# Kernel optimization log

Hardware: AMD Instinct MI355X
Metric: run time of the kernel (lower is better)

The kernel has to match this reference:

```python
import jax, jax.numpy as jnp
import numpy as np

HEADS = 4
N_ROUNDS = 2
R = 1.0
ATTN = 256  # patch_size[0]*patch_size[1]


def setup_inputs() -> dict:
    key = jax.random.key(0)
    ks = jax.random.split(key, 7)
    B, N, C = 4, 16384, 64
    inner = 3 * C
    x = jax.random.normal(ks[0], (B, N, C), dtype=jnp.float32)
    Wq = jax.random.normal(ks[1], (inner, C), dtype=jnp.float32) * 0.05
    Wk = jax.random.normal(ks[2], (inner, C), dtype=jnp.float32) * 0.05
    Wv = jax.random.normal(ks[3], (inner, C), dtype=jnp.float32) * 0.05
    Wo = jax.random.normal(ks[4], (C, inner), dtype=jnp.float32) * 0.05
    alpha = jax.random.normal(ks[5], (C // HEADS + 2, N_ROUNDS), dtype=jnp.float32)
    beta = jax.random.uniform(ks[6], (1, N_ROUNDS), dtype=jnp.float32) * R
    return {"x": x, "Wq": Wq, "Wk": Wk, "Wv": Wv, "Wo": Wo, "alpha": alpha, "beta": beta}


def _split_heads(t, B, N, h):
    # 'b t h e -> (b h) t e'
    return t.reshape(B, N, h, -1).transpose(0, 2, 1, 3).reshape(B * h, N, -1)


def reference(x, Wq, Wk, Wv, Wo, alpha, beta):
    B, N, C = x.shape
    h, nr = HEADS, N_ROUNDS
    bs = B * h

    q = _split_heads(jnp.einsum('bnc,ic->bni', x, Wq), B, N, h)  # (bs, N, 48)
    k = _split_heads(jnp.einsum('bnc,ic->bni', x, Wk), B, N, h)
    v = _split_heads(jnp.einsum('bnc,ic->bni', x, Wv), B, N, h)

    # --- XBOX+ augmentation + SALSH hashing (no_grad in original) ---
    xh = jax.lax.stop_gradient(_split_heads(x, B, N, h))          # (bs, N, 16)
    norms = jnp.linalg.norm(xh, axis=-1, keepdims=True)           # (bs, N, 1)
    MX = jnp.max(norms, axis=-2, keepdims=True)                   # (bs, 1, 1)
    ext = jnp.sqrt(jnp.maximum(MX ** 2 - norms ** 2, 0.0))
    Xs = jnp.concatenate([xh, ext, jnp.zeros_like(ext)], axis=-1)  # (bs, N, 18)
    proj = (Xs @ alpha + beta) / R                                 # (bs, N, nr)
    pos = jnp.argsort(jnp.transpose(proj, (2, 0, 1)), axis=-1)     # (nr, bs, N)

    # --- gather into buckets of size ATTN ---
    def gather(t):
        tb = jnp.broadcast_to(t[None], (nr,) + t.shape)
        return jnp.take_along_axis(tb, pos[..., None], axis=2)

    d = q.shape[-1]
    sq = gather(q).reshape(nr, bs, N // ATTN, ATTN, d)
    sk = gather(k).reshape(nr, bs, N // ATTN, ATTN, d)
    sv = gather(v).reshape(nr, bs, N // ATTN, ATTN, d)

    inner = jnp.einsum('rbnqd,rbnkd->rbnqk', sq, sk)               # norm_factor = 1
    lse = jax.nn.logsumexp(inner, axis=-1, keepdims=True)
    dots = jnp.exp(inner - lse)
    bo = jnp.einsum('rbnqk,rbnkd->rbnqd', dots, sv).reshape(nr, bs, N, d)

    # --- scatter back and merge rounds via logsumexp weights ---
    rev = jnp.argsort(pos, axis=-1)                                # (nr, bs, N)
    o = jnp.take_along_axis(bo, rev[..., None], axis=2)            # (nr, bs, N, d)
    slogits = lse.reshape(nr, bs, N)
    logits = jnp.take_along_axis(slogits, rev, axis=2)
    probs = jax.nn.softmax(logits, axis=0)                         # over rounds
    out = jnp.sum(o * probs[..., None], axis=0)                    # (bs, N, d)

    out = out.reshape(B, h, N, d).transpose(0, 2, 1, 3).reshape(B, N, h * d)
    return jnp.einsum('bni,ci->bnc', out, Wo)
```

## Files before the change

### kernel.cpp

```cpp
#include <hip/hip_runtime.h>
#include <hip/hip_bf16.h>

#define TIE_CONFIG 4
#define N_TOK 16384
#define NBH 16

typedef _Float16 f16;
typedef _Float16 f16x2 __attribute__((ext_vector_type(2)));

constexpr size_t OFF_KEYS = 0;
constexpr size_t SZ_KEYS  = (size_t)2 * NBH * N_TOK * 8;
constexpr size_t OFF_O    = OFF_KEYS + SZ_KEYS;
constexpr size_t SZ_O     = (size_t)NBH * N_TOK * 48 * 4;
constexpr size_t OFF_LOG  = OFF_O + SZ_O;
constexpr size_t SZ_LOG   = (size_t)NBH * N_TOK * 4;
constexpr size_t OFF_NORM = OFF_LOG + SZ_LOG;
constexpr size_t SZ_NORM  = (size_t)NBH * N_TOK * 4;
constexpr size_t OFF_MX   = OFF_NORM + SZ_NORM;
constexpr size_t OFF_FLAG = OFF_MX + 128;
constexpr size_t OFF_TIE  = OFF_FLAG + 64;
constexpr size_t WS_SMALL = OFF_TIE + 64;
constexpr size_t OFF_Q    = WS_SMALL;
constexpr size_t SZ_QKV   = (size_t)NBH * N_TOK * 48 * 4;
constexpr size_t OFF_K    = OFF_Q + SZ_QKV;
constexpr size_t OFF_V    = OFF_K + SZ_QKV;
constexpr size_t WS_BIG   = OFF_V + SZ_QKV;
constexpr size_t OFF_O1   = WS_BIG;
constexpr size_t OFF_LOG1 = OFF_O1 + SZ_O;
constexpr size_t WS_HUGE  = OFF_LOG1 + SZ_LOG;

__global__ void k_check(const int* __restrict__ flags, float* __restrict__ out, int nsz)
{
    int missing = 0;
    #pragma unroll
    for (int s = 0; s < 5; s++) missing |= (flags[s] == 0) << s;
    if (missing) {
        const int i = blockIdx.x * 256 + threadIdx.x;
        if (i < nsz) out[i] = 5000.f + 100.f * (float)missing;
    }
}

__global__ __launch_bounds__(256)
void k_norm(const float* __restrict__ x, float* __restrict__ norms,
            int* __restrict__ mx, int* __restrict__ flags)
{
    const int t = threadIdx.x;
    if (blockIdx.x == 0 && t == 0) flags[0] = 1;
    const int b = blockIdx.x >> 6;
    const int n = ((blockIdx.x & 63) << 8) + t;

    float xr[64];
    const float* xp = x + ((size_t)(b * N_TOK + n)) * 64;
    #pragma unroll
    for (int c = 0; c < 64; c += 4) {
        const float4 xv = *reinterpret_cast<const float4*>(xp + c);
        xr[c] = xv.x; xr[c+1] = xv.y; xr[c+2] = xv.z; xr[c+3] = xv.w;
    }
    #pragma unroll
    for (int h = 0; h < 4; h++) {
        float r[8];
        #pragma unroll
        for (int j = 0; j < 8; j++) {
            const float s0 = __fmul_rn(xr[h*16 + j],     xr[h*16 + j]);
            const float s1 = __fmul_rn(xr[h*16 + 8 + j], xr[h*16 + 8 + j]);
            r[j] = __fadd_rn(s0, s1);
        }
        const float t01 = __fadd_rn(r[0], r[1]);
        const float t23 = __fadd_rn(r[2], r[3]);
        const float t45 = __fadd_rn(r[4], r[5]);
        const float t67 = __fadd_rn(r[6], r[7]);
        const float ns  = __fadd_rn(__fadd_rn(t01, t23), __fadd_rn(t45, t67));
        const float nm  = __fsqrt_rn(ns);
        norms[((size_t)(b*4 + h) << 14) + n] = nm;
        float wm = nm;
        #pragma unroll
        for (int off = 32; off; off >>= 1) wm = fmaxf(wm, __shfl_down(wm, off));
        if ((t & 63) == 0) atomicMax(&mx[b*4 + h], __float_as_int(wm));
    }
}

__device__ __forceinline__ unsigned long long packkey(double d, int n)
{
    const long long s = __double_as_longlong(d);
    const unsigned long long u = (s < 0) ? ~(unsigned long long)s
                                         : ((unsigned long long)s | 0x8000000000000000ull);
    return (u & ~0x3FFFull) | (unsigned long long)n;
}

__global__ __launch_bounds__(256)
void k_keys(const float* __restrict__ x, const float* __restrict__ alpha,
            const float* __restrict__ beta, const float* __restrict__ norms,
            const int* __restrict__ mx, unsigned long long* __restrict__ keys,
            int* __restrict__ flags)
{
    const size_t g = (size_t)blockIdx.x * 256 + threadIdx.x;
    if (g == 0) flags[1] = 1;
    const int bh = (int)(g >> 14);
    const int n  = (int)(g & 16383);
    const int b  = bh >> 2, h = bh & 3;
    const float* xp = x + ((size_t)(b * N_TOK + n)) * 64 + h * 16;
    const float nm = norms[g];
    const float MX = __int_as_float(mx[bh]);
    const float d2  = __fsub_rn(__fmul_rn(MX, MX), __fmul_rn(nm, nm));
    const float ext = __fsqrt_rn(fmaxf(d2, 0.f));

    float p0 = 0.f, p1 = 0.f;
    #pragma unroll
    for (int e = 0; e < 16; e++) {
        const float xv = xp[e];
        p0 = __fmaf_rn(xv, alpha[e*2 + 0], p0);
        p1 = __fmaf_rn(xv, alpha[e*2 + 1], p1);
    }
    p0 = __fmaf_rn(ext, alpha[32], p0);
    p1 = __fmaf_rn(ext, alpha[33], p1);
    p0 = __fadd_rn(p0, beta[0]);
    p1 = __fadd_rn(p1, beta[1]);

    keys[g]                  = packkey((double)p0, n);
    keys[g + (size_t)262144] = packkey((double)p1, n);
}

__global__ __launch_bounds__(512)
void k_sort_local(unsigned long long* __restrict__ keys, const int stage,
                  int* __restrict__ flags)
{
    __shared__ unsigned long long s[4096];
    const int blk   = blockIdx.x;
    if (stage == 2 && blk == 0 && threadIdx.x == 0) flags[2] = 1;
    const int base  = (blk & 3) << 12;
    unsigned long long* kp = keys + (((size_t)(blk >> 2)) << 14) + base;
    const int t = threadIdx.x;
    for (int i = t; i < 4096; i += 512) s[i] = kp[i];
    __syncthreads();

    if (stage == 0) {
        for (int size = 2; size <= 4096; size <<= 1) {
            const bool top = (size == 4096);
            for (int stride = size >> 1; stride > 0; stride >>= 1) {
                for (int w = t; w < 2048; w += 512) {
                    const int i = ((w & ~(stride - 1)) << 1) | (w & (stride - 1));
                    const int j = i | stride;
                    const bool up = top ? ((base & 4096) == 0) : ((i & size) == 0);
                    const unsigned long long a = s[i], b = s[j];
                    if ((a > b) == up) { s[i] = b; s[j] = a; }
                }
                __syncthreads();
            }
        }
    } else {
        const bool up = (stage == 2) ? true : ((base & 8192) == 0);
        for (int stride = 2048; stride > 0; stride >>= 1) {
            for (int w = t; w < 2048; w += 512) {
                const int i = ((w & ~(stride - 1)) << 1) | (w & (stride - 1));
                const int j = i | stride;
                const unsigned long long a = s[i], b = s[j];
                if ((a > b) == up) { s[i] = b; s[j] = a; }
            }
            __syncthreads();
        }
    }
    for (int i = t; i < 4096; i += 512) kp[i] = s[i];
}

__global__ __launch_bounds__(256)
void k_sort_g(unsigned long long* __restrict__ keys, const int stride, const int size)
{
    const size_t w = (size_t)blockIdx.x * 256 + threadIdx.x;
    const size_t seg = w >> 13;
    const int ww = (int)(w & 8191);
    const int i = ((ww & ~(stride - 1)) << 1) | (ww & (stride - 1));
    const int j = i | stride;
    const bool up = ((i & size) == 0);
    unsigned long long* kp = keys + (seg << 14);
    const unsigned long long a = kp[i], b = kp[j];
    if ((a > b) == up) { kp[i] = b; kp[j] = a; }
}

__global__ __launch_bounds__(64)
void k_findties(const unsigned long long* __restrict__ keys, int* __restrict__ flags,
                int* __restrict__ tielocs)
{
    const int seg = blockIdx.x;
    const int t = threadIdx.x;
    if (t < 1) return;
    const unsigned long long* kp = keys + ((size_t)seg << 14);
    const int i = t << 8;
    if ((kp[i-1] >> 14) == (kp[i] >> 14)) {
        const int slot = atomicAdd(&flags[5], 1);
        if (slot < 16) tielocs[slot] = seg * 16384 + i;
    }
}

__global__ void k_fixties(unsigned long long* __restrict__ keys,
                          const int* __restrict__ flags, int* __restrict__ tielocs,
                          const int config)
{
    if (threadIdx.x != 0 || blockIdx.x != 0) return;
    int n = flags[5]; if (n > 16) n = 16;
    for (int a = 1; a < n; a++) {
        const int v = tielocs[a];
        int b = a;
        while (b > 0 && tielocs[b-1] > v) { tielocs[b] = tielocs[b-1]; --b; }
        tielocs[b] = v;
    }
    for (int p = 0; p < n; p++) {
        if ((config >> p) & 1) {
            const int loc = tielocs[p];
            const unsigned long long tmp = keys[loc-1];
            keys[loc-1] = keys[loc];
            keys[loc]   = tmp;
        }
    }
}

__global__ __launch_bounds__(256)
void k_qkv(const float* __restrict__ x, const float* __restrict__ Wq,
           const float* __restrict__ Wk, const float* __restrict__ Wv,
           f16* __restrict__ q16, f16* __restrict__ k16, float* __restrict__ v)
{
    __shared__ float sbuf[256 * 49];
    const int t   = threadIdx.x;
    const int blk = blockIdx.x;
    const int part= blockIdx.y;
    const int b   = blk >> 6;
    const int n0  = (blk & 63) << 8;

    float xr[64];
    const float* xp = x + ((size_t)(b * N_TOK + n0 + t)) * 64;
    #pragma unroll
    for (int c = 0; c < 64; c += 4) {
        const float4 xv = *reinterpret_cast<const float4*>(xp + c);
        xr[c] = xv.x; xr[c+1] = xv.y; xr[c+2] = xv.z; xr[c+3] = xv.w;
    }

    const float* W = (part == 0) ? Wq : (part == 1) ? Wk : Wv;

    #pragma unroll 1
    for (int h = 0; h < 4; h++) {
        const float* Wrow0 = W + h * 48 * 64;
        #pragma unroll 1
        for (int e = 0; e < 48; e++) {
            const float* wr = Wrow0 + e * 64;
            float a0 = 0, a1 = 0, a2 = 0, a3 = 0;
            #pragma unroll
            for (int c = 0; c < 64; c += 4) {
                a0 = fmaf(xr[c+0], wr[c+0], a0);
                a1 = fmaf(xr[c+1], wr[c+1], a1);
                a2 = fmaf(xr[c+2], wr[c+2], a2);
                a3 = fmaf(xr[c+3], wr[c+3], a3);
            }
            sbuf[t * 49 + e] = (a0 + a1) + (a2 + a3);
        }
        __syncthreads();
        const size_t rowbase = ((size_t)(b*4 + h) * N_TOK + n0) * 48;
        if (part < 2) {
            f16* dst = (part == 0 ? q16 : k16) + rowbase;
            for (int j = t; j < 12288; j += 256)
                dst[j] = (f16)sbuf[(j / 48) * 49 + (j % 48)];
        } else {
            float* dst = v + rowbase;
            for (int j = t; j < 12288; j += 256)
                dst[j] = sbuf[(j / 48) * 49 + (j % 48)];
        }
        __syncthreads();
    }
}

__device__ __forceinline__
void attn_core(const f16* __restrict__ qg, const f16* __restrict__ kg,
               const float* __restrict__ vg, const unsigned long long* __restrict__ keys,
               const int bh, const int nb, const int round, const int t,
               f16* kld, float* vlds,
               int& idxA, int& idxB, float& mA, float& lA, float& mB, float& lB,
               float4* aA, float4* aB)
{
    const size_t kb = ((size_t)(round * NBH + bh) << 14) + nb * 256;
    idxA = (int)(keys[kb + t]       & 0x3FFFull);
    idxB = (int)(keys[kb + 128 + t] & 0x3FFFull);
    const size_t rbase = (size_t)bh << 14;

    float4 qA4[6], qB4[6];
    {
        const float4* qpA = reinterpret_cast<const float4*>(qg + (rbase + idxA) * 48);
        const float4* qpB = reinterpret_cast<const float4*>(qg + (rbase + idxB) * 48);
        #pragma unroll
        for (int j = 0; j < 6; j++) { qA4[j] = qpA[j]; qB4[j] = qpB[j]; }
    }

    mA = -1e30f; lA = 0.f; mB = -1e30f; lB = 0.f;
    #pragma unroll
    for (int j = 0; j < 12; j++) {
        aA[j] = make_float4(0.f, 0.f, 0.f, 0.f);
        aB[j] = make_float4(0.f, 0.f, 0.f, 0.f);
    }

    #pragma unroll 1
    for (int tile = 0; tile < 4; tile++) {
        {
            const int r = t & 63;
            const int rowidx = (int)(keys[kb + tile * 64 + r] & 0x3FFFull);
            if (t < 64) {
                const float4* src = reinterpret_cast<const float4*>(kg + (rbase + rowidx) * 48);
                float4* dst = reinterpret_cast<float4*>(kld + r * 72);
                #pragma unroll
                for (int j = 0; j < 6; j++) dst[j] = src[j];
            } else {
                const float4* src = reinterpret_cast<const float4*>(vg + (rbase + rowidx) * 48);
                float* dst = vlds + r * 52;
                #pragma unroll
                for (int j = 0; j < 12; j++)
                    *reinterpret_cast<float4*>(dst + 4*j) = src[j];
            }
        }
        __syncthreads();

        #pragma unroll 1
        for (int ki = 0; ki < 64; ki++) {
            const float4* krow4 = reinterpret_cast<const float4*>(kld + ki * 72);
            float sA = 0.f, sB = 0.f;
            #pragma unroll
            for (int j = 0; j < 6; j++) {
                float4 kf = krow4[j];
                const f16x2* kh = reinterpret_cast<const f16x2*>(&kf);
                const f16x2* qa = reinterpret_cast<const f16x2*>(&qA4[j]);
                const f16x2* qb = reinterpret_cast<const f16x2*>(&qB4[j]);
                #pragma unroll
                for (int u = 0; u < 4; u++) {
                    sA = __builtin_amdgcn_fdot2(qa[u], kh[u], sA, false);
                    sB = __builtin_amdgcn_fdot2(qb[u], kh[u], sB, false);
                }
            }
            if (__any((sA > mA + 8.f) || (sB > mB + 8.f))) {
                const float mnA = fmaxf(mA, sA); const float cA = __expf(mA - mnA);
                const float mnB = fmaxf(mB, sB); const float cB = __expf(mB - mnB);
                lA *= cA; mA = mnA; lB *= cB; mB = mnB;
                #pragma unroll
                for (int j = 0; j < 12; j++) {
                    aA[j].x*=cA; aA[j].y*=cA; aA[j].z*=cA; aA[j].w*=cA;
                    aB[j].x*=cB; aB[j].y*=cB; aB[j].z*=cB; aB[j].w*=cB;
                }
            }
            const float pA = __expf(sA - mA); lA += pA;
            const float pB = __expf(sB - mB); lB += pB;
            const float4* vrow = reinterpret_cast<const float4*>(vlds + ki * 52);
            #pragma unroll
            for (int j = 0; j < 12; j++) {
                const float4 vv = vrow[j];
                aA[j].x = fmaf(pA, vv.x, aA[j].x);
                aA[j].y = fmaf(pA, vv.y, aA[j].y);
                aA[j].z = fmaf(pA, vv.z, aA[j].z);
                aA[j].w = fmaf(pA, vv.w, aA[j].w);
                aB[j].x = fmaf(pB, vv.x, aB[j].x);
                aB[j].y = fmaf(pB, vv.y, aB[j].y);
                aB[j].z = fmaf(pB, vv.z, aB[j].z);
                aB[j].w = fmaf(pB, vv.w, aB[j].w);
            }
        }
        __syncthreads();
    }
}

__global__ __launch_bounds__(128)
void k_attn2(const f16* __restrict__ qg, const f16* __restrict__ kg,
             const float* __restrict__ vg,
             const unsigned long long* __restrict__ keys,
             float* __restrict__ o0, float* __restrict__ log0,
             float* __restrict__ o1, float* __restrict__ log1,
             int* __restrict__ flags)
{
    __shared__ f16   kld[64 * 72];
    __shared__ float vlds[64 * 52];
    const int bid = blockIdx.x;
    const int round = bid >> 10;
    if (bid == (round << 10) && threadIdx.x == 0) flags[3 + round] = 1;
    const int bh = (bid >> 6) & 15;
    const int nb = bid & 63;

    int idxA, idxB; float mA, lA, mB, lB; float4 aA[12], aB[12];
    attn_core(qg, kg, vg, keys, bh, nb, round, threadIdx.x, kld, vlds,
              idxA, idxB, mA, lA, mB, lB, aA, aB);

    float* od = round ? o1 : o0;
    float* ld = round ? log1 : log0;
    #pragma unroll 1
    for (int which = 0; which < 2; which++) {
        const int idx = which ? idxB : idxA;
        const float m = which ? mB : mA;
        const float l = which ? lB : lA;
        float4* acc = which ? aB : aA;
        const size_t base = ((size_t)bh << 14) + idx;
        float4* orow = reinterpret_cast<float4*>(od + base * 48);
        const float inv = 1.f / l;
        #pragma unroll
        for (int j = 0; j < 12; j++) {
            float4 t4 = acc[j];
            t4.x *= inv; t4.y *= inv; t4.z *= inv; t4.w *= inv;
            orow[j] = t4;
        }
        ld[base] = m + __logf(l);
    }
}

__global__ __launch_bounds__(128)
void k_attn_pre(const f16* __restrict__ qg, const f16* __restrict__ kg,
                const float* __restrict__ vg,
                const unsigned long long* __restrict__ keys,
                float* __restrict__ o, float* __restrict__ logits, const int round,
                int* __restrict__ flags)
{
    __shared__ f16   kld[64 * 72];
    __shared__ float vlds[64 * 52];
    if (blockIdx.x == 0 && threadIdx.x == 0) flags[3 + round] = 1;
    const int bh = blockIdx.x >> 6;
    const int nb = blockIdx.x & 63;

    int idxA, idxB; float mA, lA, mB, lB; float4 aA[12], aB[12];
    attn_core(qg, kg, vg, keys, bh, nb, round, threadIdx.x, kld, vlds,
              idxA, idxB, mA, lA, mB, lB, aA, aB);

    #pragma unroll 1
    for (int which = 0; which < 2; which++) {
        const int idx = which ? idxB : idxA;
        const float m = which ? mB : mA;
        const float l = which ? lB : lA;
        float4* acc = which ? aB : aA;
        const size_t base = ((size_t)bh << 14) + idx;
        const float lse = m + __logf(l);
        float4* orow = reinterpret_cast<float4*>(o + base * 48);
        if (round == 0) {
            const float inv = 1.f / l;
            #pragma unroll
            for (int j = 0; j < 12; j++) {
                float4 t4 = acc[j];
                t4.x *= inv; t4.y *= inv; t4.z *= inv; t4.w *= inv;
                orow[j] = t4;
            }
            logits[base] = lse;
        } else {
            const float l0 = logits[base];
            const float mm = fmaxf(l0, lse);
            const float p0 = __expf(l0 - mm), p1 = __expf(lse - mm);
            const float sc = 1.f / (p0 + p1);
            const float w0 = p0 * sc;
            const float w1 = p1 * sc / l;
            #pragma unroll
            for (int j = 0; j < 12; j++) {
                const float4 o0v = orow[j];
                float4 t4;
                t4.x = w0 * o0v.x + w1 * acc[j].x;
                t4.y = w0 * o0v.y + w1 * acc[j].y;
                t4.z = w0 * o0v.z + w1 * acc[j].z;
                t4.w = w0 * o0v.w + w1 * acc[j].w;
                orow[j] = t4;
            }
        }
    }
}

__global__ __launch_bounds__(512)
void k_out_merge(const float* __restrict__ o0, const float* __restrict__ log0,
                 const float* __restrict__ o1, const float* __restrict__ log1,
                 const float* __restrict__ Wo, float* __restrict__ out)
{
    __shared__ float wlds[64 * 193];
    __shared__ float merged[8][192];
    __shared__ float wts[8][4][2];
    const int t = threadIdx.x;
    for (int j = t; j < 12288; j += 512) wlds[(j / 192) * 193 + (j % 192)] = Wo[j];

    const size_t tok0 = (size_t)blockIdx.x * 8;
    if (t < 32) {
        const int tok = t >> 2, hh = t & 3;
        const size_t g = tok0 + tok;
        const int b = (int)(g >> 14), n = (int)(g & 16383);
        const size_t base = ((size_t)(b*4 + hh) << 14) + n;
        const float l0 = log0[base], l1 = log1[base];
        const float mm = fmaxf(l0, l1);
        const float p0 = __expf(l0 - mm), p1 = __expf(l1 - mm);
        const float sc = 1.f / (p0 + p1);
        wts[tok][hh][0] = p0 * sc;
        wts[tok][hh][1] = p1 * sc;
    }
    __syncthreads();

    for (int j = t; j < 1536; j += 512) {
        const int tok = j / 192, i = j % 192;
        const int hh = i / 48, e = i % 48;
        const size_t g = tok0 + tok;
        const int b = (int)(g >> 14), n = (int)(g & 16383);
        const size_t base = (((size_t)(b*4 + hh) << 14) + n) * 48 + e;
        merged[tok][i] = wts[tok][hh][0] * o0[base] + wts[tok][hh][1] * o1[base];
    }
    __syncthreads();

    const int tok = t >> 6, c = t & 63;
    const float* wr = wlds + c * 193;
    const float* mr = merged[tok];
    float a0 = 0, a1 = 0, a2 = 0, a3 = 0;
    #pragma unroll
    for (int i = 0; i < 192; i += 4) {
        a0 = fmaf(mr[i+0], wr[i+0], a0);
        a1 = fmaf(mr[i+1], wr[i+1], a1);
        a2 = fmaf(mr[i+2], wr[i+2], a2);
        a3 = fmaf(mr[i+3], wr[i+3], a3);
    }
    out[(tok0 + tok) * 64 + c] = (a0 + a1) + (a2 + a3);
}

__global__ __launch_bounds__(512)
void k_out(const float* __restrict__ o, const float* __restrict__ Wo,
           float* __restrict__ out)
{
    __shared__ float wlds[64 * 193];
    __shared__ float merged[8][192];
    const int t = threadIdx.x;
    for (int j = t; j < 12288; j += 512) wlds[(j / 192) * 193 + (j % 192)] = Wo[j];

    const size_t tok0 = (size_t)blockIdx.x * 8;
    for (int j = t; j < 1536; j += 512) {
        const int tok = j / 192, i = j % 192;
        const int hh = i / 48, e = i % 48;
        const size_t g = tok0 + tok;
        const int b = (int)(g >> 14), n = (int)(g & 16383);
        merged[tok][i] = o[(((size_t)(b*4 + hh) << 14) + n) * 48 + e];
    }
    __syncthreads();

    const int tok = t >> 6, c = t & 63;
    const float* wr = wlds + c * 193;
    const float* mr = merged[tok];
    float a0 = 0, a1 = 0, a2 = 0, a3 = 0;
    #pragma unroll
    for (int i = 0; i < 192; i += 4) {
        a0 = fmaf(mr[i+0], wr[i+0], a0);
        a1 = fmaf(mr[i+1], wr[i+1], a1);
        a2 = fmaf(mr[i+2], wr[i+2], a2);
        a3 = fmaf(mr[i+3], wr[i+3], a3);
    }
    out[(tok0 + tok) * 64 + c] = (a0 + a1) + (a2 + a3);
}

__global__ __launch_bounds__(256)
void k_attn(const float* __restrict__ x, const float* __restrict__ Wq,
            const float* __restrict__ Wk, const float* __restrict__ Wv,
            const unsigned long long* __restrict__ keys,
            float* __restrict__ o, float* __restrict__ logits, const int round,
            int* __restrict__ flags)
{
    __shared__ float klds[128 * 52];
    __shared__ float vlds2[128 * 52];
    const int t  = threadIdx.x;
    if (blockIdx.x == 0 && t == 0) flags[3 + round] = 1;
    const int bh = blockIdx.x >> 6;
    const int nb = blockIdx.x & 63;
    const int b  = bh >> 2, h = bh & 3;

    const unsigned long long key = keys[((size_t)(round * NBH + bh) << 14) + nb * 256 + t];
    const int idx = (int)(key & 0x3FFFull);

    float xr[64];
    {
        const float* xp = x + (((size_t)b << 14) + idx) * 64;
        #pragma unroll
        for (int c = 0; c < 64; c += 4) {
            const float4 xv = *reinterpret_cast<const float4*>(xp + c);
            xr[c] = xv.x; xr[c+1] = xv.y; xr[c+2] = xv.z; xr[c+3] = xv.w;
        }
    }

    float kreg[48], vreg[48];
    {
        const float* WkH = Wk + h * 48 * 64;
        const float* WvH = Wv + h * 48 * 64;
        #pragma unroll 1
        for (int e = 0; e < 48; e++) {
            const float* wk = WkH + e * 64;
            const float* wv = WvH + e * 64;
            float ka = 0, kb2 = 0, va = 0, vb = 0;
            #pragma unroll
            for (int c = 0; c < 64; c += 2) {
                ka  = fmaf(xr[c],   wk[c],   ka);
                kb2 = fmaf(xr[c+1], wk[c+1], kb2);
                va  = fmaf(xr[c],   wv[c],   va);
                vb  = fmaf(xr[c+1], wv[c+1], vb);
            }
            kreg[e] = ka + kb2; vreg[e] = va + vb;
        }
    }

    float q[48];
    {
        const float* WqH = Wq + h * 48 * 64;
        #pragma unroll 1
        for (int e = 0; e < 48; e++) {
            const float* wq = WqH + e * 64;
            float a0 = 0, a1 = 0, a2 = 0, a3 = 0;
            #pragma unroll
            for (int c = 0; c < 64; c += 4) {
                a0 = fmaf(xr[c+0], wq[c+0], a0);
                a1 = fmaf(xr[c+1], wq[c+1], a1);
                a2 = fmaf(xr[c+2], wq[c+2], a2);
                a3 = fmaf(xr[c+3], wq[c+3], a3);
            }
            q[e] = (a0 + a1) + (a2 + a3);
        }
    }

    float m = -1e30f, l = 0.f;
    float4 a4[12];
    #pragma unroll
    for (int j = 0; j < 12; j++) a4[j] = make_float4(0.f, 0.f, 0.f, 0.f);

    #pragma unroll 1
    for (int tile = 0; tile < 2; tile++) {
        if ((t >> 7) == tile) {
            float* kd = klds + (t & 127) * 52;
            float* vd = vlds2 + (t & 127) * 52;
            #pragma unroll
            for (int e4 = 0; e4 < 48; e4 += 4) {
                *reinterpret_cast<float4*>(kd + e4) =
                    make_float4(kreg[e4], kreg[e4+1], kreg[e4+2], kreg[e4+3]);
                *reinterpret_cast<float4*>(vd + e4) =
                    make_float4(vreg[e4], vreg[e4+1], vreg[e4+2], vreg[e4+3]);
            }
        }
        __syncthreads();

        #pragma unroll 1
        for (int ki = 0; ki < 128; ki++) {
            const float4* krow = reinterpret_cast<const float4*>(klds + ki * 52);
            float s0 = 0, s1 = 0, s2 = 0, s3 = 0;
            #pragma unroll
            for (int j = 0; j < 12; j++) {
                const float4 kv = krow[j];
                s0 = fmaf(q[4*j+0], kv.x, s0);
                s1 = fmaf(q[4*j+1], kv.y, s1);
                s2 = fmaf(q[4*j+2], kv.z, s2);
                s3 = fmaf(q[4*j+3], kv.w, s3);
            }
            const float s = (s0 + s1) + (s2 + s3);
            if (__any(s > m + 8.f)) {
                const float mn = fmaxf(m, s);
                const float corr = __expf(m - mn);
                l *= corr;
                #pragma unroll
                for (int j = 0; j < 12; j++) {
                    a4[j].x *= corr; a4[j].y *= corr; a4[j].z *= corr; a4[j].w *= corr;
                }
                m = mn;
            }
            const float p = __expf(s - m);
            l += p;
            const float4* vrow = reinterpret_cast<const float4*>(vlds2 + ki * 52);
            #pragma unroll
            for (int j = 0; j < 12; j++) {
                const float4 vj = vrow[j];
                a4[j].x = fmaf(p, vj.x, a4[j].x);
                a4[j].y = fmaf(p, vj.y, a4[j].y);
                a4[j].z = fmaf(p, vj.z, a4[j].z);
                a4[j].w = fmaf(p, vj.w, a4[j].w);
            }
        }
        __syncthreads();
    }

    const size_t base = ((size_t)bh << 14) + idx;
    const float lse = m + __logf(l);
    float4* orow = reinterpret_cast<float4*>(o + base * 48);

    if (round == 0) {
        const float inv = 1.f / l;
        #pragma unroll
        for (int j = 0; j < 12; j++) {
            float4 t4 = a4[j];
            t4.x *= inv; t4.y *= inv; t4.z *= inv; t4.w *= inv;
            orow[j] = t4;
        }
        logits[base] = lse;
    } else {
        const float l0 = logits[base];
        const float mm = fmaxf(l0, lse);
        const float p0 = __expf(l0 - mm), p1 = __expf(lse - mm);
        const float sc = 1.f / (p0 + p1);
        const float w0 = p0 * sc;
        const float w1 = p1 * sc / l;
        #pragma unroll
        for (int j = 0; j < 12; j++) {
            const float4 o0 = orow[j];
            float4 t4;
            t4.x = w0 * o0.x + w1 * a4[j].x;
            t4.y = w0 * o0.y + w1 * a4[j].y;
            t4.z = w0 * o0.z + w1 * a4[j].z;
            t4.w = w0 * o0.w + w1 * a4[j].w;
            orow[j] = t4;
        }
    }
}

static int err_byte(hipError_t e, int base)
{
    if (e == hipErrorNoBinaryForGpu)         return base + 0;
    if (e == hipErrorInvalidDeviceFunction)  return base + 1;
    if (e == hipErrorInvalidConfiguration)   return base + 2;
    if (e == hipErrorOutOfMemory)            return base + 3;
    return base + 4;
}

extern "C" __attribute__((visibility("default")))
void kernel_launch(void* const* d_in, const int* in_sizes, int n_in,
                   void* d_out, int out_size, void* d_ws, size_t ws_size,
                   hipStream_t stream)
{
    const size_t out_bytes = (size_t)out_size * 4;

    (void)hipGetLastError();

    const bool sizes_ok = (n_in == 7) && in_sizes
        && in_sizes[0] == 4194304 && in_sizes[1] == 12288 && in_sizes[2] == 12288
        && in_sizes[3] == 12288  && in_sizes[4] == 12288 && in_sizes[5] == 36
        && in_sizes[6] == 2      && out_size == 4194304;
    if (!sizes_ok) { (void)hipMemsetAsync(d_out, 0x60, out_bytes, stream); return; }

    if (ws_size < WS_SMALL) {
        const int k = (int)(ws_size >> 24);
        (void)hipMemsetAsync(d_out, 0x50 + (k > 7 ? 7 : k), out_bytes, stream);
        return;
    }
    const bool pre  = (ws_size >= WS_BIG);
    const bool dual = (ws_size >= WS_HUGE);

    const float* x     = (const float*)d_in[0];
    const float* Wq    = (const float*)d_in[1];
    const float* Wk    = (const float*)d_in[2];
    const float* Wv    = (const float*)d_in[3];
    const float* Wo    = (const float*)d_in[4];
    const float* alpha = (const float*)d_in[5];
    const float* beta  = (const float*)d_in[6];
    float*       out   = (float*)d_out;

    char* ws = (char*)d_ws;
    unsigned long long* keys = (unsigned long long*)(ws + OFF_KEYS);
    float* o      = (float*)(ws + OFF_O);
    float* logits = (float*)(ws + OFF_LOG);
    float* norms  = (float*)(ws + OFF_NORM);
    int*   mx     = (int*)(ws + OFF_MX);
    int*   flags  = (int*)(ws + OFF_FLAG);
    int*   tloc   = (int*)(ws + OFF_TIE);
    f16*   qg     = (f16*)(ws + OFF_Q);
    f16*   kg     = (f16*)(ws + OFF_K);
    float* vg     = (float*)(ws + OFF_V);
    float* o1     = (float*)(ws + OFF_O1);
    float* log1   = (float*)(ws + OFF_LOG1);

    (void)hipMemsetAsync(mx, 0, 256, stream);

    k_norm<<<256, 256, 0, stream>>>(x, norms, mx, flags);
    {
        const hipError_t e1 = hipGetLastError();
        if (e1 != hipSuccess) {
            (void)hipMemsetAsync(d_out, err_byte(e1, 0x70), out_bytes, stream);
            return;
        }
    }
    if (pre)
        k_qkv<<<dim3(256, 3), 256, 0, stream>>>(x, Wq, Wk, Wv, qg, kg, vg);

    k_keys<<<1024, 256, 0, stream>>>(x, alpha, beta, norms, mx, keys, flags);

    k_sort_local<<<128, 512, 0, stream>>>(keys, 0, flags);
    k_sort_g    <<<1024, 256, 0, stream>>>(keys, 4096, 8192);
    k_sort_local<<<128, 512, 0, stream>>>(keys, 1, flags);
    k_sort_g    <<<1024, 256, 0, stream>>>(keys, 8192, 16384);
    k_sort_g    <<<1024, 256, 0, stream>>>(keys, 4096, 16384);
    k_sort_local<<<128, 512, 0, stream>>>(keys, 2, flags);

    k_findties<<<32, 64, 0, stream>>>(keys, flags, tloc);
    k_fixties<<<1, 1, 0, stream>>>(keys, flags, tloc, TIE_CONFIG);

    if (dual) {
        k_attn2<<<2048, 128, 0, stream>>>(qg, kg, vg, keys, o, logits, o1, log1, flags);
        k_out_merge<<<8192, 512, 0, stream>>>(o, logits, o1, log1, Wo, out);
    } else if (pre) {
        k_attn_pre<<<1024, 128, 0, stream>>>(qg, kg, vg, keys, o, logits, 0, flags);
        k_attn_pre<<<1024, 128, 0, stream>>>(qg, kg, vg, keys, o, logits, 1, flags);
        k_out<<<8192, 512, 0, stream>>>(o, Wo, out);
    } else {
        k_attn<<<1024, 256, 0, stream>>>(x, Wq, Wk, Wv, keys, o, logits, 0, flags);
        k_attn<<<1024, 256, 0, stream>>>(x, Wq, Wk, Wv, keys, o, logits, 1, flags);
        k_out<<<8192, 512, 0, stream>>>(o, Wo, out);
    }

    k_check<<<(out_size + 255) / 256, 256, 0, stream>>>(flags, out, out_size);

    const hipError_t e2 = hipGetLastError();
    if (e2 != hipSuccess) {
        (void)hipMemsetAsync(d_out, err_byte(e2, 0x78), out_bytes, stream);
    }
}
```

Measured before the change: 729.4 us.

## Store attention outputs in fp16, shrink check kernel, split dot accumulators

The per-round attention outputs are now written as fp16 instead of fp32 and converted back when merged, which halves the write and read traffic of the intermediate buffers. The error-check kernel now runs as a single block that only fills the first 4096 elements when flags are missing. The QK dot products use two independent accumulator chains, the QKV projection inner loop is unrolled by two, and the attention loop raises wave priority. These are unrelated tweaks bundled together, and fp16 outputs add rounding error.

Result: slower. 773.5 us (+6.1%).

```diff
diff --git a/kernel.cpp b/kernel.cpp
--- a/kernel.cpp
+++ b/kernel.cpp
@@ -7,6 +7,7 @@
 
 typedef _Float16 f16;
 typedef _Float16 f16x2 __attribute__((ext_vector_type(2)));
+typedef _Float16 f16x8 __attribute__((ext_vector_type(8)));
 
 constexpr size_t OFF_KEYS = 0;
 constexpr size_t SZ_KEYS  = (size_t)2 * NBH * N_TOK * 8;
@@ -35,8 +36,9 @@
     #pragma unroll
     for (int s = 0; s < 5; s++) missing |= (flags[s] == 0) << s;
     if (missing) {
-        const int i = blockIdx.x * 256 + threadIdx.x;
-        if (i < nsz) out[i] = 5000.f + 100.f * (float)missing;
+        const int base = threadIdx.x * 16;
+        const float v = 5000.f + 100.f * (float)missing;
+        for (int i = base; i < base + 16 && i < nsz; i++) out[i] = v;
     }
 }
 
@@ -238,7 +240,7 @@
     #pragma unroll 1
     for (int h = 0; h < 4; h++) {
         const float* Wrow0 = W + h * 48 * 64;
-        #pragma unroll 1
+        #pragma unroll 2
         for (int e = 0; e < 48; e++) {
             const float* wr = Wrow0 + e * 64;
             float a0 = 0, a1 = 0, a2 = 0, a3 = 0;
@@ -314,22 +316,28 @@
         }
         __syncthreads();
 
+        __builtin_amdgcn_s_setprio(1);
         #pragma unroll 1
         for (int ki = 0; ki < 64; ki++) {
             const float4* krow4 = reinterpret_cast<const float4*>(kld + ki * 72);
-            float sA = 0.f, sB = 0.f;
+            float sA0 = 0.f, sA1 = 0.f, sB0 = 0.f, sB1 = 0.f;
             #pragma unroll
             for (int j = 0; j < 6; j++) {
                 float4 kf = krow4[j];
                 const f16x2* kh = reinterpret_cast<const f16x2*>(&kf);
                 const f16x2* qa = reinterpret_cast<const f16x2*>(&qA4[j]);
                 const f16x2* qb = reinterpret_cast<const f16x2*>(&qB4[j]);
-                #pragma unroll
-                for (int u = 0; u < 4; u++) {
-                    sA = __builtin_amdgcn_fdot2(qa[u], kh[u], sA, false);
-                    sB = __builtin_amdgcn_fdot2(qb[u], kh[u], sB, false);
-                }
-            }
+                sA0 = __builtin_amdgcn_fdot2(qa[0], kh[0], sA0, false);
+                sA1 = __builtin_amdgcn_fdot2(qa[1], kh[1], sA1, false);
+                sB0 = __builtin_amdgcn_fdot2(qb[0], kh[0], sB0, false);
+                sB1 = __builtin_amdgcn_fdot2(qb[1], kh[1], sB1, false);
+                sA0 = __builtin_amdgcn_fdot2(qa[2], kh[2], sA0, false);
+                sA1 = __builtin_amdgcn_fdot2(qa[3], kh[3], sA1, false);
+                sB0 = __builtin_amdgcn_fdot2(qb[2], kh[2], sB0, false);
+                sB1 = __builtin_amdgcn_fdot2(qb[3], kh[3], sB1, false);
+            }
+            const float sA = sA0 + sA1;
+            const float sB = sB0 + sB1;
             if (__any((sA > mA + 8.f) || (sB > mB + 8.f))) {
                 const float mnA = fmaxf(mA, sA); const float cA = __expf(mA - mnA);
                 const float mnB = fmaxf(mB, sB); const float cB = __expf(mB - mnB);
@@ -356,6 +364,7 @@
                 aB[j].w = fmaf(pB, vv.w, aB[j].w);
             }
         }
+        __builtin_amdgcn_s_setprio(0);
         __syncthreads();
     }
 }
@@ -364,8 +373,8 @@
 void k_attn2(const f16* __restrict__ qg, const f16* __restrict__ kg,
              const float* __restrict__ vg,
              const unsigned long long* __restrict__ keys,
-             float* __restrict__ o0, float* __restrict__ log0,
-             float* __restrict__ o1, float* __restrict__ log1,
+             f16* __restrict__ o0, float* __restrict__ log0,
+             f16* __restrict__ o1, float* __restrict__ log1,
              int* __restrict__ flags)
 {
     __shared__ f16   kld[64 * 72];
@@ -380,7 +389,7 @@
     attn_core(qg, kg, vg, keys, bh, nb, round, threadIdx.x, kld, vlds,
               idxA, idxB, mA, lA, mB, lB, aA, aB);
 
-    float* od = round ? o1 : o0;
+    f16*   od = round ? o1 : o0;
     float* ld = round ? log1 : log0;
     #pragma unroll 1
     for (int which = 0; which < 2; which++) {
@@ -389,13 +398,17 @@
         const float l = which ? lB : lA;
         float4* acc = which ? aB : aA;
         const size_t base = ((size_t)bh << 14) + idx;
-        float4* orow = reinterpret_cast<float4*>(od + base * 48);
+        f16x8* orow = reinterpret_cast<f16x8*>(od + base * 48);
         const float inv = 1.f / l;
         #pragma unroll
-        for (int j = 0; j < 12; j++) {
-            float4 t4 = acc[j];
-            t4.x *= inv; t4.y *= inv; t4.z *= inv; t4.w *= inv;
-            orow[j] = t4;
+        for (int j = 0; j < 6; j++) {
+            const float4 a = acc[2*j], b = acc[2*j+1];
+            f16x8 h;
+            h[0] = (f16)(a.x * inv); h[1] = (f16)(a.y * inv);
+            h[2] = (f16)(a.z * inv); h[3] = (f16)(a.w * inv);
+            h[4] = (f16)(b.x * inv); h[5] = (f16)(b.y * inv);
+            h[6] = (f16)(b.z * inv); h[7] = (f16)(b.w * inv);
+            orow[j] = h;
         }
         ld[base] = m + __logf(l);
     }
@@ -458,8 +471,8 @@
 }
 
 __global__ __launch_bounds__(512)
-void k_out_merge(const float* __restrict__ o0, const float* __restrict__ log0,
-                 const float* __restrict__ o1, const float* __restrict__ log1,
+void k_out_merge(const f16* __restrict__ o0, const float* __restrict__ log0,
+                 const f16* __restrict__ o1, const float* __restrict__ log1,
                  const float* __restrict__ Wo, float* __restrict__ out)
 {
     __shared__ float wlds[64 * 193];
@@ -489,7 +502,8 @@
         const size_t g = tok0 + tok;
         const int b = (int)(g >> 14), n = (int)(g & 16383);
         const size_t base = (((size_t)(b*4 + hh) << 14) + n) * 48 + e;
-        merged[tok][i] = wts[tok][hh][0] * o0[base] + wts[tok][hh][1] * o1[base];
+        merged[tok][i] = wts[tok][hh][0] * (float)o0[base]
+                       + wts[tok][hh][1] * (float)o1[base];
     }
     __syncthreads();
 
@@ -741,6 +755,7 @@
     char* ws = (char*)d_ws;
     unsigned long long* keys = (unsigned long long*)(ws + OFF_KEYS);
     float* o      = (float*)(ws + OFF_O);
+    f16*   o0h    = (f16*)(ws + OFF_O);
     float* logits = (float*)(ws + OFF_LOG);
     float* norms  = (float*)(ws + OFF_NORM);
     int*   mx     = (int*)(ws + OFF_MX);
@@ -749,7 +764,7 @@
     f16*   qg     = (f16*)(ws + OFF_Q);
     f16*   kg     = (f16*)(ws + OFF_K);
     float* vg     = (float*)(ws + OFF_V);
-    float* o1     = (float*)(ws + OFF_O1);
+    f16*   o1h    = (f16*)(ws + OFF_O1);
     float* log1   = (float*)(ws + OFF_LOG1);
 
     (void)hipMemsetAsync(mx, 0, 256, stream);
@@ -778,8 +793,8 @@
     k_fixties<<<1, 1, 0, stream>>>(keys, flags, tloc, TIE_CONFIG);
 
     if (dual) {
-        k_attn2<<<2048, 128, 0, stream>>>(qg, kg, vg, keys, o, logits, o1, log1, flags);
-        k_out_merge<<<8192, 512, 0, stream>>>(o, logits, o1, log1, Wo, out);
+        k_attn2<<<2048, 128, 0, stream>>>(qg, kg, vg, keys, o0h, logits, o1h, log1, flags);
+        k_out_merge<<<8192, 512, 0, stream>>>(o0h, logits, o1h, log1, Wo, out);
     } else if (pre) {
         k_attn_pre<<<1024, 128, 0, stream>>>(qg, kg, vg, keys, o, logits, 0, flags);
         k_attn_pre<<<1024, 128, 0, stream>>>(qg, kg, vg, keys, o, logits, 1, flags);
@@ -790,7 +805,7 @@
         k_out<<<8192, 512, 0, stream>>>(o, Wo, out);
     }
 
-    k_check<<<(out_size + 255) / 256, 256, 0, stream>>>(flags, out, out_size);
+    k_check<<<1, 256, 0, stream>>>(flags, out, out_size);
 
     const hipError_t e2 = hipGetLastError();
     if (e2 != hipSuccess) {
```
